# Kernel optimization log

Hardware: AMD Instinct MI355X
Metric: run time of the kernel (lower is better)

## Reference

```python
import jax, jax.numpy as jnp
import numpy as np

DIM = 512
H = 8
D = 64
EPS = 1e-5


def _ln(x, g, b):
    m = jnp.mean(x, axis=-1, keepdims=True)
    v = jnp.var(x, axis=-1, keepdims=True)
    return (x - m) * jax.lax.rsqrt(v + EPS) * g + b


def _attn(x, ctx, wq, wk, wv, wo, bo):
    B, S, _ = x.shape
    T = ctx.shape[1]
    q = (x @ wq).reshape(B, S, H, D)
    k = (ctx @ wk).reshape(B, T, H, D)
    v = (ctx @ wv).reshape(B, T, H, D)
    scale = D ** -0.5
    score = jnp.einsum('bqhd,bkhd->bhqk', q, k) * scale  # [B,H,S,T]
    w = jax.nn.softmax(score, axis=-1)
    o = jnp.einsum('bhqk,bkhd->bqhd', w, v).reshape(B, S, H * D)
    return o @ wo + bo


def _geglu(x, w, b):
    h = x @ w + b
    y, gate = h[..., :4 * DIM], h[..., 4 * DIM:]
    tanh_res = jnp.tanh(gate * 0.7978845608 * (1.0 + 0.044715 * gate * gate))
    return y * 0.5 * gate * (1.0 + tanh_res)


def setup_inputs() -> dict:
    key = jax.random.key(0)
    ks = jax.random.split(key, 16)
    s = 0.02
    inp = {
        'x': jax.random.normal(ks[0], (2, 4096, DIM), jnp.float32),
        'context': jax.random.normal(ks[1], (2, 77, DIM), jnp.float32),
        'ln1_g': jnp.ones((DIM,), jnp.float32),
        'ln1_b': jnp.zeros((DIM,), jnp.float32),
        'wq1': jax.random.normal(ks[2], (DIM, H * D), jnp.float32) * s,
        'wk1': jax.random.normal(ks[3], (DIM, H * D), jnp.float32) * s,
        'wv1': jax.random.normal(ks[4], (DIM, H * D), jnp.float32) * s,
        'wo1': jax.random.normal(ks[5], (H * D, H * D), jnp.float32) * s,
        'bo1': jnp.zeros((H * D,), jnp.float32),
        'ln2_g': jnp.ones((DIM,), jnp.float32),
        'ln2_b': jnp.zeros((DIM,), jnp.float32),
        'wq2': jax.random.normal(ks[6], (DIM, H * D), jnp.float32) * s,
        'wk2': jax.random.normal(ks[7], (DIM, H * D), jnp.float32) * s,
        'wv2': jax.random.normal(ks[8], (DIM, H * D), jnp.float32) * s,
        'wo2': jax.random.normal(ks[9], (H * D, H * D), jnp.float32) * s,
        'bo2': jnp.zeros((H * D,), jnp.float32),
        'ln3_g': jnp.ones((DIM,), jnp.float32),
        'ln3_b': jnp.zeros((DIM,), jnp.float32),
        'geglu_w': jax.random.normal(ks[10], (DIM, 8 * DIM), jnp.float32) * s,
        'geglu_b': jnp.zeros((8 * DIM,), jnp.float32),
        'out_w': jax.random.normal(ks[11], (4 * DIM, DIM), jnp.float32) * s,
        'out_b': jnp.zeros((DIM,), jnp.float32),
    }
    return inp


def reference(x, context, ln1_g, ln1_b, wq1, wk1, wv1, wo1, bo1,
              ln2_g, ln2_b, wq2, wk2, wv2, wo2, bo2,
              ln3_g, ln3_b, geglu_w, geglu_b, out_w, out_b):
    h = _attn(_ln(x, ln1_g, ln1_b), _ln(x, ln1_g, ln1_b), wq1, wk1, wv1, wo1, bo1) + x
    h = _attn(_ln(h, ln2_g, ln2_b), context, wq2, wk2, wv2, wo2, bo2) + h
    ff = _geglu(_ln(h, ln3_g, ln3_b), geglu_w, geglu_b)
    return ff @ out_w + out_b + h
```

## Files before the change

kernel.cpp:

```cpp
#include <hip/hip_runtime.h>
#include <hip/hip_bf16.h>
#include <math.h>

#define DIM 512
#define NHEAD 8
#define HD 64
#define BATCH 2
#define SEQ 4096
#define CTXLEN 77
#define NTOK (BATCH*SEQ)
#define NCTX (BATCH*CTXLEN)

typedef __hip_bfloat16 bf16;
typedef __attribute__((ext_vector_type(8))) short bf8_t;
typedef __attribute__((ext_vector_type(4))) float f4_t;

__device__ __forceinline__ float b2f(bf16 v){ return __bfloat162float(v); }
__device__ __forceinline__ bf16  f2b(float v){ return __float2bfloat16(v); }
__device__ __forceinline__ unsigned short f2bu(float v){ bf16 h = f2b(v); return *(unsigned short*)&h; }
__device__ __forceinline__ unsigned int packbf2(float a, float b){
    unsigned int au = __float_as_uint(a) + 0x8000u;
    unsigned int bu = __float_as_uint(b) + 0x8000u;
    return __builtin_amdgcn_perm(bu, au, 0x07060302u);
}
__device__ __forceinline__ void  stf(float* p, float v){ *p = v; }
__device__ __forceinline__ void  stf(bf16* p, float v){ *p = f2b(v); }

__global__ __launch_bounds__(256)
void ln_kernel(const float* __restrict__ x, const float* __restrict__ g,
               const float* __restrict__ b, bf16* __restrict__ out, int nrows)
{
    int row  = blockIdx.x * 4 + (threadIdx.x >> 6);
    int lane = threadIdx.x & 63;
    if (row >= nrows) return;
    const float* xr = x + (size_t)row * DIM;
    float v[8];
    float s = 0.f, sq = 0.f;
    #pragma unroll
    for (int j = 0; j < 8; ++j) {
        float f = xr[lane + 64*j];
        v[j] = f; s += f; sq += f*f;
    }
    #pragma unroll
    for (int off = 32; off; off >>= 1) {
        s  += __shfl_xor(s,  off);
        sq += __shfl_xor(sq, off);
    }
    float mean = s * (1.f/DIM);
    float var  = sq * (1.f/DIM) - mean*mean;
    float rstd = rsqrtf(var + 1e-5f);
    bf16* orow = out + (size_t)row * DIM;
    #pragma unroll
    for (int j = 0; j < 8; ++j) {
        int c = lane + 64*j;
        orow[c] = f2b((v[j]-mean)*rstd*g[c] + b[c]);
    }
}

__global__ __launch_bounds__(256)
void transpose_bf16_kernel(const float* __restrict__ W, bf16* __restrict__ Wt, int K, int N)
{
    __shared__ float tile[32][33];
    int n0 = blockIdx.x * 32, k0 = blockIdx.y * 32;
    int tx = threadIdx.x & 31, ty = threadIdx.x >> 5;
    #pragma unroll
    for (int p = 0; p < 4; ++p)
        tile[ty + p*8][tx] = W[(size_t)(k0 + ty + p*8)*N + n0 + tx];
    __syncthreads();
    #pragma unroll
    for (int p = 0; p < 4; ++p)
        Wt[(size_t)(n0 + ty + p*8)*K + k0 + tx] = f2b(tile[tx][ty + p*8]);
}

struct TPtrs { const float* src[8]; bf16* dst[8]; };
__global__ __launch_bounds__(256)
void transpose8_kernel(TPtrs p)
{
    __shared__ float tile[32][33];
    const float* W = p.src[blockIdx.z];
    bf16* Wt = p.dst[blockIdx.z];
    int n0 = blockIdx.x * 32, k0 = blockIdx.y * 32;
    int tx = threadIdx.x & 31, ty = threadIdx.x >> 5;
    #pragma unroll
    for (int q = 0; q < 4; ++q)
        tile[ty + q*8][tx] = W[(size_t)(k0 + ty + q*8)*512 + n0 + tx];
    __syncthreads();
    #pragma unroll
    for (int q = 0; q < 4; ++q)
        Wt[(size_t)(n0 + ty + q*8)*512 + k0 + tx] = f2b(tile[tx][ty + q*8]);
}

__global__ __launch_bounds__(256)
void cast_bf16_kernel(const float* __restrict__ in, bf16* __restrict__ out, int n)
{
    int i = blockIdx.x*256 + threadIdx.x;
    if (i < n) out[i] = f2b(in[i]);
}

__global__ __launch_bounds__(256)
void v_transpose_kernel(const bf16* __restrict__ V, bf16* __restrict__ Vt, int T, int pitch)
{
    __shared__ __align__(16) unsigned short tile[64*64];
    const int tid = threadIdx.x;
    const int b = blockIdx.z, h = blockIdx.y;
    const int t0 = blockIdx.x * 64;
    #pragma unroll
    for (int it = 0; it < 2; ++it) {
        int e = tid + it*256;
        int t = e >> 3, c = e & 7;
        int gk = t0 + t;
        bf8_t v = {0,0,0,0,0,0,0,0};
        if (gk < T) v = *(const bf8_t*)(V + ((size_t)(b*T + gk))*DIM + h*HD + c*8);
        *(bf8_t*)&tile[t*64 + c*8] = v;
    }
    __syncthreads();
    #pragma unroll
    for (int it = 0; it < 2; ++it) {
        int e = tid + it*256;
        int d = e & 63, oc = e >> 6;
        unsigned short tmp[8];
        #pragma unroll
        for (int j = 0; j < 8; ++j) tmp[j] = tile[(oc*8 + j)*64 + d];
        *(bf8_t*)(Vt + ((size_t)((b*8 + h)*64 + d))*pitch + t0 + oc*8) = *(bf8_t*)tmp;
    }
}

struct OutPtrs { void* p[3]; };
template<int RESID, typename OUTT, bool GUARD>
__global__ __launch_bounds__(256)
void gemm_mfma_kernel(const bf16* __restrict__ A, const bf16* __restrict__ Wt,
                      const float* __restrict__ bias, const float* __restrict__ resid,
                      OutPtrs outs, int M, int K)
{
    __shared__ __align__(16) unsigned short As[128*64];
    __shared__ __align__(16) unsigned short Bs[64*64];
    const int tid  = threadIdx.x;
    const int wave = tid >> 6, lane = tid & 63;
    const int l16  = lane & 15, quad = lane >> 4;
    const int wm = (wave >> 1) * 64, wn = (wave & 1) * 32;
    const int m0 = blockIdx.y * 128, n0 = blockIdx.x * 64;
    OUTT* outp = (OUTT*)outs.p[n0 >> 9];
    const int lc0 = n0 & 511;
    const int sr = tid >> 3, sc_ = tid & 7;

    f4_t acc[4][2];
    #pragma unroll
    for (int i = 0; i < 4; ++i) { acc[i][0] = f4_t{0,0,0,0}; acc[i][1] = f4_t{0,0,0,0}; }

    bf8_t pa[4], pb[2];
    #pragma unroll
    for (int p = 0; p < 4; ++p) {
        int r = sr + p*32;
        int gr = m0 + r;
        if (GUARD) gr = (gr < M) ? gr : (M-1);
        pa[p] = *(const bf8_t*)(A + (size_t)gr*K + sc_*8);
    }
    #pragma unroll
    for (int p = 0; p < 2; ++p)
        pb[p] = *(const bf8_t*)(Wt + (size_t)(n0 + sr + p*32)*K + sc_*8);

    for (int k0 = 0; k0 < K; k0 += 64) {
        #pragma unroll
        for (int p = 0; p < 4; ++p) {
            int r = sr + p*32;
            *(bf8_t*)&As[r*64 + ((sc_ ^ (r&7))*8)] = pa[p];
        }
        #pragma unroll
        for (int p = 0; p < 2; ++p) {
            int r = sr + p*32;
            *(bf8_t*)&Bs[r*64 + ((sc_ ^ (r&7))*8)] = pb[p];
        }
        __syncthreads();
        if (k0 + 64 < K) {
            #pragma unroll
            for (int p = 0; p < 4; ++p) {
                int r = sr + p*32;
                int gr = m0 + r;
                if (GUARD) gr = (gr < M) ? gr : (M-1);
                pa[p] = *(const bf8_t*)(A + (size_t)gr*K + k0 + 64 + sc_*8);
            }
            #pragma unroll
            for (int p = 0; p < 2; ++p)
                pb[p] = *(const bf8_t*)(Wt + (size_t)(n0 + sr + p*32)*K + k0 + 64 + sc_*8);
        }
        #pragma unroll
        for (int kc = 0; kc < 2; ++kc) {
            const int cg = kc*4 + quad;
            bf8_t af[4], bfr[2];
            #pragma unroll
            for (int mt = 0; mt < 4; ++mt) {
                int r = wm + mt*16 + l16;
                af[mt] = *(const bf8_t*)&As[r*64 + ((cg ^ (r&7))*8)];
            }
            #pragma unroll
            for (int nt = 0; nt < 2; ++nt) {
                int r = wn + nt*16 + l16;
                bfr[nt] = *(const bf8_t*)&Bs[r*64 + ((cg ^ (r&7))*8)];
            }
            #pragma unroll
            for (int mt = 0; mt < 4; ++mt)
                #pragma unroll
                for (int nt = 0; nt < 2; ++nt)
                    acc[mt][nt] = __builtin_amdgcn_mfma_f32_16x16x32_bf16(af[mt], bfr[nt], acc[mt][nt], 0, 0, 0);
        }
        __syncthreads();
    }

    #pragma unroll
    for (int mt = 0; mt < 4; ++mt) {
        #pragma unroll
        for (int r_ = 0; r_ < 4; ++r_) {
            int row = m0 + wm + mt*16 + quad*4 + r_;
            if (GUARD && row >= M) continue;
            size_t rb = (size_t)row * 512;
            #pragma unroll
            for (int nt = 0; nt < 2; ++nt) {
                int col = lc0 + wn + nt*16 + l16;
                float v = acc[mt][nt][r_];
                if (bias) v += bias[col];
                if (RESID) v += resid[rb + col];
                stf(&outp[rb + col], v);
            }
        }
    }
}

__global__ __launch_bounds__(256)
void geglu_mfma_kernel(const bf16* __restrict__ A, const bf16* __restrict__ WtG,
                       const float* __restrict__ bias, bf16* __restrict__ outp)
{
    __shared__ __align__(16) unsigned short As[128*64];
    __shared__ __align__(16) unsigned short Bys[64*64];
    __shared__ __align__(16) unsigned short Bgs[64*64];
    const int tid  = threadIdx.x;
    const int wave = tid >> 6, lane = tid & 63;
    const int l16  = lane & 15, quad = lane >> 4;
    const int m0 = blockIdx.y * 128, n0 = blockIdx.x * 64;
    const int sr = tid >> 3, sc_ = tid & 7;

    f4_t accy[2][4], accg[2][4];
    #pragma unroll
    for (int i = 0; i < 2; ++i)
        #pragma unroll
        for (int j = 0; j < 4; ++j) { accy[i][j] = f4_t{0,0,0,0}; accg[i][j] = f4_t{0,0,0,0}; }

    bf8_t pa[4], py[2], pg[2];
    #pragma unroll
    for (int p = 0; p < 4; ++p)
        pa[p] = *(const bf8_t*)(A + (size_t)(m0 + sr + p*32)*DIM + sc_*8);
    #pragma unroll
    for (int p = 0; p < 2; ++p) {
        py[p] = *(const bf8_t*)(WtG + (size_t)(n0 + sr + p*32)*DIM + sc_*8);
        pg[p] = *(const bf8_t*)(WtG + (size_t)(2048 + n0 + sr + p*32)*DIM + sc_*8);
    }

    for (int k0 = 0; k0 < DIM; k0 += 64) {
        #pragma unroll
        for (int p = 0; p < 4; ++p) {
            int r = sr + p*32;
            *(bf8_t*)&As[r*64 + ((sc_ ^ (r&7))*8)] = pa[p];
        }
        #pragma unroll
        for (int p = 0; p < 2; ++p) {
            int r = sr + p*32;
            *(bf8_t*)&Bys[r*64 + ((sc_ ^ (r&7))*8)] = py[p];
            *(bf8_t*)&Bgs[r*64 + ((sc_ ^ (r&7))*8)] = pg[p];
        }
        __syncthreads();
        if (k0 + 64 < DIM) {
            #pragma unroll
            for (int p = 0; p < 4; ++p)
                pa[p] = *(const bf8_t*)(A + (size_t)(m0 + sr + p*32)*DIM + k0 + 64 + sc_*8);
            #pragma unroll
            for (int p = 0; p < 2; ++p) {
                py[p] = *(const bf8_t*)(WtG + (size_t)(n0 + sr + p*32)*DIM + k0 + 64 + sc_*8);
                pg[p] = *(const bf8_t*)(WtG + (size_t)(2048 + n0 + sr + p*32)*DIM + k0 + 64 + sc_*8);
            }
        }
        #pragma unroll
        for (int kc = 0; kc < 2; ++kc) {
            const int cg = kc*4 + quad;
            bf8_t af[2];
            #pragma unroll
            for (int mt = 0; mt < 2; ++mt) {
                int r = wave*32 + mt*16 + l16;
                af[mt] = *(const bf8_t*)&As[r*64 + ((cg ^ (r&7))*8)];
            }
            #pragma unroll
            for (int nt = 0; nt < 4; ++nt) {
                int r = nt*16 + l16;
                bf8_t by = *(const bf8_t*)&Bys[r*64 + ((cg ^ (r&7))*8)];
                bf8_t bg = *(const bf8_t*)&Bgs[r*64 + ((cg ^ (r&7))*8)];
                #pragma unroll
                for (int mt = 0; mt < 2; ++mt) {
                    accy[mt][nt] = __builtin_amdgcn_mfma_f32_16x16x32_bf16(af[mt], by, accy[mt][nt], 0, 0, 0);
                    accg[mt][nt] = __builtin_amdgcn_mfma_f32_16x16x32_bf16(af[mt], bg, accg[mt][nt], 0, 0, 0);
                }
            }
        }
        __syncthreads();
    }

    #pragma unroll
    for (int mt = 0; mt < 2; ++mt) {
        #pragma unroll
        for (int r_ = 0; r_ < 4; ++r_) {
            int row = m0 + wave*32 + mt*16 + quad*4 + r_;
            size_t rb = (size_t)row * 2048;
            #pragma unroll
            for (int nt = 0; nt < 4; ++nt) {
                int col = n0 + nt*16 + l16;
                float y = accy[mt][nt][r_] + bias[col];
                float g = accg[mt][nt][r_] + bias[2048 + col];
                float t = tanhf(0.7978845608f*g*(1.f + 0.044715f*g*g));
                outp[rb + col] = f2b(y * 0.5f * g * (1.f + t));
            }
        }
    }
}

__global__ __launch_bounds__(512)
void attn_mfma_kernel(const bf16* __restrict__ Qm, const bf16* __restrict__ Km,
                      const bf16* __restrict__ VtG, bf16* __restrict__ Om,
                      int T, int vpitch)
{
    __shared__ __align__(16) unsigned short Ks[2][64*64];
    __shared__ __align__(16) unsigned short Vts[2][64*64];

    const int tid  = threadIdx.x;
    const int wave = tid >> 6, lane = tid & 63;
    const int l16  = lane & 15, quad = lane >> 4;
    const int b = blockIdx.z, h = blockIdx.y;
    const int qblk = blockIdx.x * 128;
    const int sr = tid >> 3, sc_ = tid & 7;

    bf8_t ones;
    #pragma unroll
    for (int j = 0; j < 8; ++j) ((unsigned short*)&ones)[j] = 0x3F80;

    bf8_t qf[2];
    {
        const bf16* qp = Qm + ((size_t)(b*SEQ + qblk + wave*16 + l16))*DIM + h*HD + quad*8;
        #pragma unroll
        for (int kc = 0; kc < 2; ++kc) {
            bf8_t v = *(const bf8_t*)(qp + kc*32);
            unsigned short* u = (unsigned short*)&v;
            unsigned int* w = (unsigned int*)&v;
            #pragma unroll
            for (int j = 0; j < 4; ++j) {
                float f0 = b2f(*(bf16*)&u[2*j])   * 0.1803368801f;
                float f1 = b2f(*(bf16*)&u[2*j+1]) * 0.1803368801f;
                w[j] = packbf2(f0, f1);
            }
            qf[kc] = v;
        }
    }

    f4_t o[4];
    #pragma unroll
    for (int dt = 0; dt < 4; ++dt) o[dt] = f4_t{0,0,0,0};
    f4_t lacc = {0,0,0,0};

    bf8_t kq, vq;
    kq = bf8_t{0,0,0,0,0,0,0,0};
    if (sr < T) kq = *(const bf8_t*)(Km + ((size_t)(b*T + sr))*DIM + h*HD + sc_*8);
    vq = *(const bf8_t*)(VtG + ((size_t)((b*8 + h)*64 + sr))*vpitch + sc_*8);
    *(bf8_t*)&Ks[0][sr*64 + ((sc_ ^ (sr&7))*8)]  = kq;
    *(bf8_t*)&Vts[0][sr*64 + ((sc_ ^ (sr&7))*8)] = vq;
    __syncthreads();

    const int ntiles = (T + 63) >> 6;
    for (int t0 = 0; t0 < ntiles; ++t0) {
        const int kb = t0 << 6;
        const int cur = t0 & 1;
        const bool havenext = (t0 + 1 < ntiles);
        if (havenext) {
            int gk = kb + 64 + sr;
            kq = bf8_t{0,0,0,0,0,0,0,0};
            if (gk < T) kq = *(const bf8_t*)(Km + ((size_t)(b*T + gk))*DIM + h*HD + sc_*8);
            vq = *(const bf8_t*)(VtG + ((size_t)((b*8 + h)*64 + sr))*vpitch + kb + 64 + sc_*8);
        }

        bf8_t kf[4][2], vf[4][2];
        #pragma unroll
        for (int t = 0; t < 4; ++t) {
            int r = t*16 + l16;
            #pragma unroll
            for (int kc = 0; kc < 2; ++kc) {
                int cg = kc*4 + quad;
                kf[t][kc] = *(const bf8_t*)&Ks[cur][r*64 + ((cg ^ (r&7))*8)];
                vf[t][kc] = *(const bf8_t*)&Vts[cur][r*64 + ((cg ^ (r&7))*8)];
            }
        }
        const bool tail = (kb + 64 > T);

        f4_t sc4[4];
        #pragma unroll
        for (int km = 0; km < 4; ++km) {
            f4_t c = {0,0,0,0};
            c = __builtin_amdgcn_mfma_f32_16x16x32_bf16(kf[km][0], qf[0], c, 0, 0, 0);
            c = __builtin_amdgcn_mfma_f32_16x16x32_bf16(kf[km][1], qf[1], c, 0, 0, 0);
            sc4[km] = c;
        }
        if (tail) {
            #pragma unroll
            for (int km = 0; km < 4; ++km)
                #pragma unroll
                for (int r = 0; r < 4; ++r)
                    if (kb + km*16 + quad*4 + r >= T) sc4[km][r] = -1e30f;
        }
        unsigned int pk[4][2];
        #pragma unroll
        for (int km = 0; km < 4; ++km) {
            pk[km][0] = packbf2(exp2f(sc4[km][0]), exp2f(sc4[km][1]));
            pk[km][1] = packbf2(exp2f(sc4[km][2]), exp2f(sc4[km][3]));
        }
        #pragma unroll
        for (int kc = 0; kc < 2; ++kc) {
            auto s0 = __builtin_amdgcn_permlane32_swap(pk[2*kc][0], pk[2*kc+1][0], false, false);
            auto w02 = __builtin_amdgcn_permlane16_swap(s0[0], s0[1], false, false);
            auto s1 = __builtin_amdgcn_permlane32_swap(pk[2*kc][1], pk[2*kc+1][1], false, false);
            auto w13 = __builtin_amdgcn_permlane16_swap(s1[0], s1[1], false, false);
            union { unsigned int u[4]; bf8_t v; } pfu;
            pfu.u[0] = w02[0]; pfu.u[1] = w13[0]; pfu.u[2] = w02[1]; pfu.u[3] = w13[1];
            bf8_t pf = pfu.v;
            lacc = __builtin_amdgcn_mfma_f32_16x16x32_bf16(ones, pf, lacc, 0, 0, 0);
            #pragma unroll
            for (int dt = 0; dt < 4; ++dt)
                o[dt] = __builtin_amdgcn_mfma_f32_16x16x32_bf16(vf[dt][kc], pf, o[dt], 0, 0, 0);
        }
        if (havenext) {
            *(bf8_t*)&Ks[cur^1][sr*64 + ((sc_ ^ (sr&7))*8)]  = kq;
            *(bf8_t*)&Vts[cur^1][sr*64 + ((sc_ ^ (sr&7))*8)] = vq;
            __syncthreads();
        }
    }

    {
        float inv = 1.f / lacc[0];
        int tok = qblk + wave*16 + l16;
        size_t base = ((size_t)(b*SEQ + tok))*DIM + h*HD;
        #pragma unroll
        for (int dt = 0; dt < 4; ++dt) {
            uint2 w;
            w.x = packbf2(o[dt][0]*inv, o[dt][1]*inv);
            w.y = packbf2(o[dt][2]*inv, o[dt][3]*inv);
            *(uint2*)(Om + base + dt*16 + quad*4) = w;
        }
    }
}

extern "C" void kernel_launch(void* const* d_in, const int* in_sizes, int n_in,
                              void* d_out, int out_size, void* d_ws, size_t ws_size,
                              hipStream_t stream)
{
    (void)in_sizes; (void)n_in; (void)out_size; (void)ws_size;
    const float* x    = (const float*)d_in[0];
    const float* ctx  = (const float*)d_in[1];
    const float* ln1g = (const float*)d_in[2];
    const float* ln1b = (const float*)d_in[3];
    const float* wq1  = (const float*)d_in[4];
    const float* wk1  = (const float*)d_in[5];
    const float* wv1  = (const float*)d_in[6];
    const float* wo1  = (const float*)d_in[7];
    const float* bo1  = (const float*)d_in[8];
    const float* ln2g = (const float*)d_in[9];
    const float* ln2b = (const float*)d_in[10];
    const float* wq2  = (const float*)d_in[11];
    const float* wk2  = (const float*)d_in[12];
    const float* wv2  = (const float*)d_in[13];
    const float* wo2  = (const float*)d_in[14];
    const float* bo2  = (const float*)d_in[15];
    const float* ln3g = (const float*)d_in[16];
    const float* ln3b = (const float*)d_in[17];
    const float* gw   = (const float*)d_in[18];
    const float* gb   = (const float*)d_in[19];
    const float* ow   = (const float*)d_in[20];
    const float* ob   = (const float*)d_in[21];
    float* out = (float*)d_out;

    char* ws = (char*)d_ws;
    bf16* An  = (bf16*)(ws);
    bf16* VtG = (bf16*)(ws);
    bf16* Qb  = (bf16*)(ws + ((size_t)8<<20));
    bf16* Kb  = (bf16*)(ws + ((size_t)16<<20));
    bf16* Vb  = (bf16*)(ws + ((size_t)24<<20));
    bf16* Ob  = (bf16*)(ws + ((size_t)32<<20));
    bf16* FF  = Qb;
    float* Hf = out;
    bf16* WT  = (bf16*)(ws + ((size_t)40<<20));
    bf16* wq1T = WT + 0*262144, *wk1T = WT + 1*262144, *wv1T = WT + 2*262144, *wo1T = WT + 3*262144;
    bf16* wq2T = WT + 4*262144, *wk2T = WT + 5*262144, *wv2T = WT + 6*262144, *wo2T = WT + 7*262144;
    bf16* gwT  = (bf16*)(ws + ((size_t)44<<20));
    bf16* owT  = (bf16*)(ws + ((size_t)48<<20));
    bf16* ctxb = (bf16*)(ws + ((size_t)50<<20));
    bf16* VtG2 = (bf16*)(ws + ((size_t)50<<20) + ((size_t)512<<10));

    dim3 blk(256);
    dim3 blkA(512);

    TPtrs tp;
    tp.src[0]=wq1; tp.src[1]=wk1; tp.src[2]=wv1; tp.src[3]=wo1;
    tp.src[4]=wq2; tp.src[5]=wk2; tp.src[6]=wv2; tp.src[7]=wo2;
    tp.dst[0]=wq1T; tp.dst[1]=wk1T; tp.dst[2]=wv1T; tp.dst[3]=wo1T;
    tp.dst[4]=wq2T; tp.dst[5]=wk2T; tp.dst[6]=wv2T; tp.dst[7]=wo2T;
    transpose8_kernel<<<dim3(16,16,8), blk, 0, stream>>>(tp);
    transpose_bf16_kernel<<<dim3(128,16), blk, 0, stream>>>(gw, gwT, DIM, 4096);
    transpose_bf16_kernel<<<dim3(16,64), blk, 0, stream>>>(ow, owT, 2048, DIM);
    cast_bf16_kernel<<<dim3((NCTX*DIM+255)/256), blk, 0, stream>>>(ctx, ctxb, NCTX*DIM);

    dim3 gLN(NTOK/4);
    dim3 gQKV(24, 64);
    dim3 gG(8, 64);
    dim3 gKVx(16, 2);
    dim3 gGEGLU(32, 64);
    dim3 gATT(SEQ/128, NHEAD, BATCH);
    OutPtrs oQKV{{Qb, Kb, Vb}};
    OutPtrs oKVx{{Kb, Vb, nullptr}};
    OutPtrs oQ{{Qb, nullptr, nullptr}};
    OutPtrs oH{{Hf, nullptr, nullptr}};
    OutPtrs oOut{{out, nullptr, nullptr}};

    ln_kernel<<<gLN, blk, 0, stream>>>(x, ln1g, ln1b, An, NTOK);
    gemm_mfma_kernel<0,bf16,false><<<gQKV, blk, 0, stream>>>(An, wq1T, nullptr, nullptr, oQKV, NTOK, DIM);
    v_transpose_kernel<<<dim3(SEQ/64, NHEAD, BATCH), blk, 0, stream>>>(Vb, VtG, SEQ, SEQ);
    attn_mfma_kernel<<<gATT, blkA, 0, stream>>>(Qb, Kb, VtG, Ob, SEQ, SEQ);
    gemm_mfma_kernel<1,float,false><<<gG, blk, 0, stream>>>(Ob, wo1T, bo1, x, oH, NTOK, DIM);

    ln_kernel<<<gLN, blk, 0, stream>>>(Hf, ln2g, ln2b, An, NTOK);
    gemm_mfma_kernel<0,bf16,false><<<gG, blk, 0, stream>>>(An, wq2T, nullptr, nullptr, oQ, NTOK, DIM);
    gemm_mfma_kernel<0,bf16,true><<<gKVx, blk, 0, stream>>>(ctxb, wk2T, nullptr, nullptr, oKVx, NCTX, DIM);
    v_transpose_kernel<<<dim3(2, NHEAD, BATCH), blk, 0, stream>>>(Vb, VtG2, CTXLEN, 128);
    attn_mfma_kernel<<<gATT, blkA, 0, stream>>>(Qb, Kb, VtG2, Ob, CTXLEN, 128);
    gemm_mfma_kernel<1,float,false><<<gG, blk, 0, stream>>>(Ob, wo2T, bo2, Hf, oH, NTOK, DIM);

    ln_kernel<<<gLN, blk, 0, stream>>>(Hf, ln3g, ln3b, An, NTOK);
    geglu_mfma_kernel<<<gGEGLU, blk, 0, stream>>>(An, gwT, gb, FF);
    gemm_mfma_kernel<1,float,false><<<gG, blk, 0, stream>>>(FF, owT, ob, Hf, oOut, NTOK, 2048);
}
```

Measured before the change: 468.1 us.

## Stage GEMM, GEGLU and attention tiles with direct global-to-LDS loads

Replaces the register-staged global loads followed by LDS stores with `global_load_lds` DMA in three kernels, so tiles go straight from global memory into pre-swizzled shared memory. The projection GEMM gains a double-buffered LDS layout so the next K tile is fetched while the current one feeds MFMA. Attention K/V staging uses the same path, clamping out-of-range key rows instead of zero-filling them. The GEGLU kernel loses its register prefetch and becomes load-then-compute per tile, which may expose latency. The GEMM's doubled LDS use may also lower occupancy.

```diff
diff --git a/kernel.cpp b/kernel.cpp
--- a/kernel.cpp
+++ b/kernel.cpp
@@ -17,7 +17,6 @@
 
 __device__ __forceinline__ float b2f(bf16 v){ return __bfloat162float(v); }
 __device__ __forceinline__ bf16  f2b(float v){ return __float2bfloat16(v); }
-__device__ __forceinline__ unsigned short f2bu(float v){ bf16 h = f2b(v); return *(unsigned short*)&h; }
 __device__ __forceinline__ unsigned int packbf2(float a, float b){
     unsigned int au = __float_as_uint(a) + 0x8000u;
     unsigned int bu = __float_as_uint(b) + 0x8000u;
@@ -25,6 +24,13 @@
 }
 __device__ __forceinline__ void  stf(float* p, float v){ *p = v; }
 __device__ __forceinline__ void  stf(bf16* p, float v){ *p = f2b(v); }
+
+__device__ __forceinline__ void glds16(const bf16* g, unsigned short* l){
+    __builtin_amdgcn_global_load_lds(
+        (__attribute__((address_space(1))) void*)g,
+        (__attribute__((address_space(3))) void*)l,
+        16, 0, 0);
+}
 
 __global__ __launch_bounds__(256)
 void ln_kernel(const float* __restrict__ x, const float* __restrict__ g,
@@ -132,8 +138,8 @@
                       const float* __restrict__ bias, const float* __restrict__ resid,
                       OutPtrs outs, int M, int K)
 {
-    __shared__ __align__(16) unsigned short As[128*64];
-    __shared__ __align__(16) unsigned short Bs[64*64];
+    __shared__ __align__(16) unsigned short As[2][128*64];
+    __shared__ __align__(16) unsigned short Bs[2][64*64];
     const int tid  = threadIdx.x;
     const int wave = tid >> 6, lane = tid & 63;
     const int l16  = lane & 15, quad = lane >> 4;
@@ -141,48 +147,34 @@
     const int m0 = blockIdx.y * 128, n0 = blockIdx.x * 64;
     OUTT* outp = (OUTT*)outs.p[n0 >> 9];
     const int lc0 = n0 & 511;
-    const int sr = tid >> 3, sc_ = tid & 7;
+    const int lr = lane >> 3;
+    const int lc = (lane & 7) ^ lr;
 
     f4_t acc[4][2];
     #pragma unroll
     for (int i = 0; i < 4; ++i) { acc[i][0] = f4_t{0,0,0,0}; acc[i][1] = f4_t{0,0,0,0}; }
 
-    bf8_t pa[4], pb[2];
-    #pragma unroll
-    for (int p = 0; p < 4; ++p) {
-        int r = sr + p*32;
-        int gr = m0 + r;
-        if (GUARD) gr = (gr < M) ? gr : (M-1);
-        pa[p] = *(const bf8_t*)(A + (size_t)gr*K + sc_*8);
-    }
-    #pragma unroll
-    for (int p = 0; p < 2; ++p)
-        pb[p] = *(const bf8_t*)(Wt + (size_t)(n0 + sr + p*32)*K + sc_*8);
+    auto stage = [&](int k0, int bf) {
+        #pragma unroll
+        for (int i = 0; i < 4; ++i) {
+            int r = (wave*4 + i)*8 + lr;
+            int gr = m0 + r;
+            if (GUARD) gr = (gr < M) ? gr : (M-1);
+            glds16(A + (size_t)gr*K + k0 + lc*8, &As[bf][(wave*4 + i)*512]);
+        }
+        #pragma unroll
+        for (int j = 0; j < 2; ++j) {
+            int r = (wave*2 + j)*8 + lr;
+            glds16(Wt + (size_t)(n0 + r)*K + k0 + lc*8, &Bs[bf][(wave*2 + j)*512]);
+        }
+    };
+
+    stage(0, 0);
+    __syncthreads();
 
     for (int k0 = 0; k0 < K; k0 += 64) {
-        #pragma unroll
-        for (int p = 0; p < 4; ++p) {
-            int r = sr + p*32;
-            *(bf8_t*)&As[r*64 + ((sc_ ^ (r&7))*8)] = pa[p];
-        }
-        #pragma unroll
-        for (int p = 0; p < 2; ++p) {
-            int r = sr + p*32;
-            *(bf8_t*)&Bs[r*64 + ((sc_ ^ (r&7))*8)] = pb[p];
-        }
-        __syncthreads();
-        if (k0 + 64 < K) {
-            #pragma unroll
-            for (int p = 0; p < 4; ++p) {
-                int r = sr + p*32;
-                int gr = m0 + r;
-                if (GUARD) gr = (gr < M) ? gr : (M-1);
-                pa[p] = *(const bf8_t*)(A + (size_t)gr*K + k0 + 64 + sc_*8);
-            }
-            #pragma unroll
-            for (int p = 0; p < 2; ++p)
-                pb[p] = *(const bf8_t*)(Wt + (size_t)(n0 + sr + p*32)*K + k0 + 64 + sc_*8);
-        }
+        const int bf = (k0 >> 6) & 1;
+        if (k0 + 64 < K) stage(k0 + 64, bf ^ 1);
         #pragma unroll
         for (int kc = 0; kc < 2; ++kc) {
             const int cg = kc*4 + quad;
@@ -190,12 +182,12 @@
             #pragma unroll
             for (int mt = 0; mt < 4; ++mt) {
                 int r = wm + mt*16 + l16;
-                af[mt] = *(const bf8_t*)&As[r*64 + ((cg ^ (r&7))*8)];
+                af[mt] = *(const bf8_t*)&As[bf][r*64 + ((cg ^ (r&7))*8)];
             }
             #pragma unroll
             for (int nt = 0; nt < 2; ++nt) {
                 int r = wn + nt*16 + l16;
-                bfr[nt] = *(const bf8_t*)&Bs[r*64 + ((cg ^ (r&7))*8)];
+                bfr[nt] = *(const bf8_t*)&Bs[bf][r*64 + ((cg ^ (r&7))*8)];
             }
             #pragma unroll
             for (int mt = 0; mt < 4; ++mt)
@@ -236,7 +228,8 @@
     const int wave = tid >> 6, lane = tid & 63;
     const int l16  = lane & 15, quad = lane >> 4;
     const int m0 = blockIdx.y * 128, n0 = blockIdx.x * 64;
-    const int sr = tid >> 3, sc_ = tid & 7;
+    const int lr = lane >> 3;
+    const int lc = (lane & 7) ^ lr;
 
     f4_t accy[2][4], accg[2][4];
     #pragma unroll
@@ -244,39 +237,19 @@
         #pragma unroll
         for (int j = 0; j < 4; ++j) { accy[i][j] = f4_t{0,0,0,0}; accg[i][j] = f4_t{0,0,0,0}; }
 
-    bf8_t pa[4], py[2], pg[2];
-    #pragma unroll
-    for (int p = 0; p < 4; ++p)
-        pa[p] = *(const bf8_t*)(A + (size_t)(m0 + sr + p*32)*DIM + sc_*8);
-    #pragma unroll
-    for (int p = 0; p < 2; ++p) {
-        py[p] = *(const bf8_t*)(WtG + (size_t)(n0 + sr + p*32)*DIM + sc_*8);
-        pg[p] = *(const bf8_t*)(WtG + (size_t)(2048 + n0 + sr + p*32)*DIM + sc_*8);
-    }
-
     for (int k0 = 0; k0 < DIM; k0 += 64) {
         #pragma unroll
-        for (int p = 0; p < 4; ++p) {
-            int r = sr + p*32;
-            *(bf8_t*)&As[r*64 + ((sc_ ^ (r&7))*8)] = pa[p];
-        }
-        #pragma unroll
-        for (int p = 0; p < 2; ++p) {
-            int r = sr + p*32;
-            *(bf8_t*)&Bys[r*64 + ((sc_ ^ (r&7))*8)] = py[p];
-            *(bf8_t*)&Bgs[r*64 + ((sc_ ^ (r&7))*8)] = pg[p];
+        for (int i = 0; i < 4; ++i) {
+            int r = (wave*4 + i)*8 + lr;
+            glds16(A + (size_t)(m0 + r)*DIM + k0 + lc*8, &As[(wave*4 + i)*512]);
+        }
+        #pragma unroll
+        for (int j = 0; j < 2; ++j) {
+            int r = (wave*2 + j)*8 + lr;
+            glds16(WtG + (size_t)(n0 + r)*DIM + k0 + lc*8, &Bys[(wave*2 + j)*512]);
+            glds16(WtG + (size_t)(2048 + n0 + r)*DIM + k0 + lc*8, &Bgs[(wave*2 + j)*512]);
         }
         __syncthreads();
-        if (k0 + 64 < DIM) {
-            #pragma unroll
-            for (int p = 0; p < 4; ++p)
-                pa[p] = *(const bf8_t*)(A + (size_t)(m0 + sr + p*32)*DIM + k0 + 64 + sc_*8);
-            #pragma unroll
-            for (int p = 0; p < 2; ++p) {
-                py[p] = *(const bf8_t*)(WtG + (size_t)(n0 + sr + p*32)*DIM + k0 + 64 + sc_*8);
-                pg[p] = *(const bf8_t*)(WtG + (size_t)(2048 + n0 + sr + p*32)*DIM + k0 + 64 + sc_*8);
-            }
-        }
         #pragma unroll
         for (int kc = 0; kc < 2; ++kc) {
             const int cg = kc*4 + quad;
@@ -332,7 +305,9 @@
     const int l16  = lane & 15, quad = lane >> 4;
     const int b = blockIdx.z, h = blockIdx.y;
     const int qblk = blockIdx.x * 128;
-    const int sr = tid >> 3, sc_ = tid & 7;
+    const int lr = lane >> 3;
+    const int lc = (lane & 7) ^ lr;
+    const int srow = wave*8 + lr;
 
     bf8_t ones;
     #pragma unroll
@@ -361,24 +336,24 @@
     for (int dt = 0; dt < 4; ++dt) o[dt] = f4_t{0,0,0,0};
     f4_t lacc = {0,0,0,0};
 
-    bf8_t kq, vq;
-    kq = bf8_t{0,0,0,0,0,0,0,0};
-    if (sr < T) kq = *(const bf8_t*)(Km + ((size_t)(b*T + sr))*DIM + h*HD + sc_*8);
-    vq = *(const bf8_t*)(VtG + ((size_t)((b*8 + h)*64 + sr))*vpitch + sc_*8);
-    *(bf8_t*)&Ks[0][sr*64 + ((sc_ ^ (sr&7))*8)]  = kq;
-    *(bf8_t*)&Vts[0][sr*64 + ((sc_ ^ (sr&7))*8)] = vq;
+    const bf16* Kbase = Km + (size_t)b*T*DIM + h*HD;
+    const bf16* Vbase = VtG + ((size_t)((b*8 + h)*64 + srow))*vpitch;
+
+    {
+        int gk = srow; if (gk > T-1) gk = T-1;
+        glds16(Kbase + (size_t)gk*DIM + lc*8, &Ks[0][wave*512]);
+        glds16(Vbase + lc*8,                  &Vts[0][wave*512]);
+    }
     __syncthreads();
 
     const int ntiles = (T + 63) >> 6;
     for (int t0 = 0; t0 < ntiles; ++t0) {
         const int kb = t0 << 6;
         const int cur = t0 & 1;
-        const bool havenext = (t0 + 1 < ntiles);
-        if (havenext) {
-            int gk = kb + 64 + sr;
-            kq = bf8_t{0,0,0,0,0,0,0,0};
-            if (gk < T) kq = *(const bf8_t*)(Km + ((size_t)(b*T + gk))*DIM + h*HD + sc_*8);
-            vq = *(const bf8_t*)(VtG + ((size_t)((b*8 + h)*64 + sr))*vpitch + kb + 64 + sc_*8);
+        if (t0 + 1 < ntiles) {
+            int gk = kb + 64 + srow; if (gk > T-1) gk = T-1;
+            glds16(Kbase + (size_t)gk*DIM + lc*8,  &Ks[cur^1][wave*512]);
+            glds16(Vbase + kb + 64 + lc*8,         &Vts[cur^1][wave*512]);
         }
 
         bf8_t kf[4][2], vf[4][2];
@@ -429,11 +404,7 @@
             for (int dt = 0; dt < 4; ++dt)
                 o[dt] = __builtin_amdgcn_mfma_f32_16x16x32_bf16(vf[dt][kc], pf, o[dt], 0, 0, 0);
         }
-        if (havenext) {
-            *(bf8_t*)&Ks[cur^1][sr*64 + ((sc_ ^ (sr&7))*8)]  = kq;
-            *(bf8_t*)&Vts[cur^1][sr*64 + ((sc_ ^ (sr&7))*8)] = vq;
-            __syncthreads();
-        }
+        __syncthreads();
     }
 
     {
```

Result: no change. 472.2 us (+0.9%).
